# Performance work log

Measured on AMD Instinct MI355X. Metric: run time of the kernel, lower is better.

Reference implementation:

```python
import jax, jax.numpy as jnp
import numpy as np

# ---- config (from init_kwargs) ----
PRE_NMS_THRESH = 0.05
PRE_NMS_TOP_N = 1000
NMS_THRESH = 0.6
FPN_POST_NMS_TOP_N = 100
MIN_SIZE = 0.0
FPN_STRIDES = (8.0, 16.0, 32.0, 64.0, 128.0)
TO_REMOVE = 1.0

M = 2097152   # total FPN points over the batch
N = 16        # images
C = 11        # classes incl. background column (zeroed)


def setup_inputs() -> dict:
    key = jax.random.key(0)
    k1, k2, k3, k4, k5, k6 = jax.random.split(key, 6)
    locations = jax.random.uniform(k1, (M, 2), jnp.float32) * 1024.0
    box_cls = jax.random.normal(k2, (M, C), jnp.float32) * 2.0
    box_regression = jax.random.uniform(k3, (M, 4), jnp.float32) * 4.0
    centerness = jax.random.normal(k4, (M, 1), jnp.float32)
    levels = jax.random.randint(k5, (M,), 0, len(FPN_STRIDES), jnp.int32)
    batch_indices = jnp.sort(jax.random.randint(k6, (M,), 0, N, jnp.int32))
    image_sizes = jnp.tile(jnp.array([[800, 1333]], jnp.int32), (N, 1))  # (h, w)
    return dict(locations=locations, levels=levels, batch_indices=batch_indices,
                box_cls=box_cls, box_regression=box_regression,
                centerness=centerness, image_sizes=image_sizes)


def _iou_matrix(b):
    x1, y1, x2, y2 = b[:, 0], b[:, 1], b[:, 2], b[:, 3]
    area = jnp.clip(x2 - x1 + TO_REMOVE, 0.0) * jnp.clip(y2 - y1 + TO_REMOVE, 0.0)
    xx1 = jnp.maximum(x1[:, None], x1[None, :])
    yy1 = jnp.maximum(y1[:, None], y1[None, :])
    xx2 = jnp.minimum(x2[:, None], x2[None, :])
    yy2 = jnp.minimum(y2[:, None], y2[None, :])
    inter = jnp.clip(xx2 - xx1 + TO_REMOVE, 0.0) * jnp.clip(yy2 - yy1 + TO_REMOVE, 0.0)
    return inter / jnp.maximum(area[:, None] + area[None, :] - inter, 1e-9)


def _greedy_nms(iou, keep0):
    # boxes assumed sorted by descending score; keep0 = validity mask
    K = keep0.shape[0]
    idx = jnp.arange(K)
    def step(keep, i):
        sup = (iou[i] > NMS_THRESH) & (idx > i) & keep[i]
        return keep & ~sup, None
    keep, _ = jax.lax.scan(step, keep0, jnp.arange(K))
    return keep


def _fcos_post(locations, box_cls, box_regression, centerness,
               levels, batch_indices, image_sizes):
    strides = jnp.asarray(FPN_STRIDES, box_regression.dtype)
    reg = box_regression * strides[levels][:, None]          # norm_reg_targets=True
    scores = jax.nn.sigmoid(box_cls) * jax.nn.sigmoid(centerness)  # [M,C]
    scores = scores.at[:, -1].set(0.0)                       # kill background column
    boxes_all = jnp.concatenate([locations - reg[:, :2],
                                 locations + reg[:, 2:]], axis=-1)  # [M,4]

    def per_image(args):
        i, hw = args
        m = (batch_indices == i)[:, None] & (scores > PRE_NMS_THRESH)
        flat = jnp.where(m, scores, 0.0).reshape(-1)          # [M*C]
        topv, topi = jax.lax.top_k(flat, PRE_NMS_TOP_N)       # sorted desc
        pt = topi // C
        cl = (topi % C + 1).astype(jnp.int32)                 # labels = class + 1
        b = boxes_all[pt]                                     # [K,4]
        v0 = topv > 0.0                                       # pad entries -> invalid
        sc = jnp.sqrt(jnp.where(v0, topv, 1.0)) * v0          # sqrt(score), safe at pads
        h = hw[0].astype(b.dtype); w = hw[1].astype(b.dtype)
        x1 = jnp.clip(b[:, 0], 0.0, w - TO_REMOVE)            # clip_to_image
        y1 = jnp.clip(b[:, 1], 0.0, h - TO_REMOVE)
        x2 = jnp.clip(b[:, 2], 0.0, w - TO_REMOVE)
        y2 = jnp.clip(b[:, 3], 0.0, h - TO_REMOVE)
        b = jnp.stack([x1, y1, x2, y2], axis=-1)
        ws = x2 - x1 + TO_REMOVE; hs = y2 - y1 + TO_REMOVE    # remove_small_boxes
        keep0 = v0 & (ws >= MIN_SIZE) & (hs >= MIN_SIZE)
        # class-aware NMS via coordinate offset trick
        max_coord = jnp.max(jnp.where(keep0[:, None], b, 0.0))
        boff = jax.lax.stop_gradient(b + (cl.astype(b.dtype) * (max_coord + 1.0))[:, None])
        keep = _greedy_nms(_iou_matrix(boff), keep0)
        sck = jnp.where(keep, sc, 0.0)
        fv, fi = jax.lax.top_k(sck, FPN_POST_NMS_TOP_N)       # fpn_post_nms_top_n
        return b[fi], fv, cl[fi], fv > 0.0

    boxes_o, scores_o, labels_o, valid_o = jax.lax.map(
        per_image, (jnp.arange(N), image_sizes))
    return boxes_o, scores_o, labels_o, valid_o


def reference(locations, levels, batch_indices, box_cls, box_regression,
              centerness, image_sizes):
    return _fcos_post(locations, box_cls, box_regression, centerness,
                      levels, batch_indices, image_sizes)
```

## Files before the change

kernel.cpp:

```cpp
#include <hip/hip_runtime.h>
#include <math.h>

#pragma clang fp contract(off)

#define MPTS   2097152
#define NIMG   16
#define NCLS   11
#define CUTB   0x3F000000u
#define PREB   0x3F4CCC00u
#define BSAFE  620
#define PRECAP 14336
#define NB2    1026
#define NB2P   1040
#define MARG   96u
#define CAP    4096
#define TOPN   1000
#define OUTN   100
#define LCAP   64

typedef unsigned long long u64;

#define SUPW_PER_IMG 8704
__device__ __forceinline__ int chunk_base(int c) {
    return 64 * (16 * c - (c * (c - 1)) / 2);
}

__device__ inline float sigx(float x) {
    float e = (float)exp(-(double)x);
    return 1.0f / (1.0f + e);
}
__device__ inline float sigf(float x) {
    float e = __expf(-x);
    return __builtin_amdgcn_rcpf(1.0f + e);
}
__device__ inline float bfr(float x) {
    unsigned u = __float_as_uint(x);
    unsigned r = (u + 0x7FFFu + ((u >> 16) & 1u)) & 0xFFFF0000u;
    return __uint_as_float(r);
}
__device__ __forceinline__ u64 rdlane64(u64 v, int l) {
    unsigned lo = (unsigned)__builtin_amdgcn_readlane((int)(unsigned)(v & 0xFFFFFFFFull), l);
    unsigned hi = (unsigned)__builtin_amdgcn_readlane((int)(unsigned)(v >> 32), l);
    return ((u64)hi << 32) | (u64)lo;
}

__global__ __launch_bounds__(1024)
void k_hist(const float4* __restrict__ cls4, const float* __restrict__ ctr,
            const int* __restrict__ batch, unsigned* __restrict__ ghist,
            unsigned* __restrict__ gcnt, unsigned* __restrict__ prerec) {
    __shared__ unsigned hist[NB2];
    __shared__ unsigned pA[512], pB[256];
    __shared__ unsigned cA, cB, bA;
    __shared__ int simg;
    const int F4  = MPTS * NCLS / 4;
    const int FPB = F4 / 512;
    int f0 = blockIdx.x * FPB;
    int t = threadIdx.x;
    for (int i = t; i < NB2; i += 1024) hist[i] = 0;
    if (t == 0) { simg = batch[(unsigned)(4u * (unsigned)f0) / NCLS]; cA = 0; cB = 0; }
    __syncthreads();
    int bi = simg;
    unsigned pc = 0xFFFFFFFFu;
    float sfc = 0.0f;
    int bc = 0;
    for (int f = f0 + t; f < f0 + FPB; f += 1024) {
        float4 v = cls4[f];
        float va[4] = {v.x, v.y, v.z, v.w};
        unsigned e0 = 4u * (unsigned)f;
        #pragma unroll
        for (int j = 0; j < 4; j++) {
            float ck = va[j];
            if (ck <= 0.0f) continue;
            unsigned e = e0 + (unsigned)j;
            unsigned p = e / NCLS;
            unsigned k = e - p * NCLS;
            if (k == 10u) continue;
            if (p != pc) {
                pc = p; sfc = sigf(ctr[p]); bc = batch[p];
            }
            unsigned fb = __float_as_uint(sigf(ck) * sfc);
            if (fb < CUTB) continue;
            unsigned bin = (fb - CUTB) >> 13;
            if (bin >= NB2) bin = NB2 - 1;
            if (bc == bi) atomicAdd(&hist[bin], 1u);
            else          atomicAdd(&ghist[(size_t)bc * NB2P + bin], 1u);
            if (fb >= PREB) {
                if (bc == bi) {
                    unsigned sl = atomicAdd(&cA, 1u);
                    if (sl < 512u) pA[sl] = e;
                    else {
                        unsigned pos = atomicAdd(&gcnt[bi * 16 + 8], 1u);
                        if (pos < PRECAP) prerec[(size_t)bi * PRECAP + pos] = e;
                    }
                } else {
                    unsigned sl = atomicAdd(&cB, 1u);
                    if (sl < 256u) pB[sl] = e;
                    else {
                        unsigned pos = atomicAdd(&gcnt[bc * 16 + 8], 1u);
                        if (pos < PRECAP) prerec[(size_t)bc * PRECAP + pos] = e;
                    }
                }
            }
        }
    }
    __syncthreads();
    unsigned* gh = ghist + (size_t)bi * NB2P;
    for (int i = t; i < NB2; i += 1024) {
        unsigned v2 = hist[i];
        if (v2) atomicAdd(&gh[i], v2);
    }
    if (t == 0) {
        unsigned nn = cA; if (nn > 512u) nn = 512u;
        cA = nn;
        bA = nn ? atomicAdd(&gcnt[bi * 16 + 8], nn) : 0u;
    }
    __syncthreads();
    for (unsigned i = t; i < cA; i += 1024) {
        unsigned pos = bA + i;
        if (pos < PRECAP) prerec[(size_t)bi * PRECAP + pos] = pA[i];
    }
    unsigned nb = cB; if (nb > 256u) nb = 256u;
    for (unsigned i = t; i < nb; i += 1024) {
        unsigned e2 = pB[i];
        int img2 = batch[e2 / NCLS];
        unsigned pos = atomicAdd(&gcnt[img2 * 16 + 8], 1u);
        if (pos < PRECAP) prerec[(size_t)img2 * PRECAP + pos] = e2;
    }
}

__global__ void k_thresh(const unsigned* __restrict__ ghist, unsigned* __restrict__ thrbuf,
                         unsigned* __restrict__ gcnt) {
    int img = blockIdx.x;
    const unsigned* h = ghist + (size_t)img * NB2P;
    __shared__ unsigned psum[256];
    int t = threadIdx.x;
    unsigned s = 0;
    int base = t * 5;
    for (int i = 0; i < 5; i++) { int b = base + i; if (b < NB2) s += h[b]; }
    psum[t] = s;
    __syncthreads();
    if (t == 0) {
        unsigned run = 0; int B = 0;
        for (int u = 205; u >= 0; u--) {
            if (run + psum[u] >= (unsigned)TOPN) {
                int btop = u * 5 + 4; if (btop > NB2 - 1) btop = NB2 - 1;
                for (int b = btop; b >= u * 5; b--) {
                    run += h[b];
                    if (run >= (unsigned)TOPN) { B = b; break; }
                }
                break;
            }
            run += psum[u];
        }
        unsigned TB = CUTB + ((unsigned)B << 13) - MARG;
        thrbuf[2 * img] = TB;
        thrbuf[2 * img + 1] = __float_as_uint(__uint_as_float(TB) * 0.998f);
        if (B < BSAFE || gcnt[img * 16 + 8] > PRECAP) atomicOr(&gcnt[1], 1u);
    }
}

__global__ __launch_bounds__(256)
void k_collect(const float4* __restrict__ cls4, const float* __restrict__ clsf,
               const float* __restrict__ ctr, const int* __restrict__ batch,
               const unsigned* __restrict__ thrbuf, unsigned* __restrict__ gcnt,
               const unsigned* __restrict__ prerec, unsigned long long* __restrict__ cand) {
    int t = threadIdx.x;
    if (gcnt[1] == 0u) {
        if (blockIdx.x >= 256) return;
        int img = blockIdx.x >> 4;
        int sub = blockIdx.x & 15;
        unsigned TB = thrbuf[2 * img];
        float scr = __uint_as_float(thrbuf[2 * img + 1]);
        unsigned n = gcnt[img * 16 + 8];
        __shared__ u64 l2[512];
        __shared__ unsigned c2, b2;
        if (t == 0) c2 = 0;
        __syncthreads();
        const unsigned* pr = prerec + (size_t)img * PRECAP;
        for (unsigned i = (unsigned)(sub * 256 + t); i < n; i += 4096) {
            unsigned e = pr[i];
            unsigned p = e / NCLS;
            float ck = clsf[e];
            float cgs = ctr[p];
            float sf = sigf(ck) * sigf(cgs);
            if (sf > scr) {
                float s = sigx(ck) * sigx(cgs);
                unsigned bits = __float_as_uint(s);
                if (bits >= TB && s > 0.05f) {
                    u64 key = ((u64)bits << 32) | (u64)(0xFFFFFFFFu - e);
                    unsigned sl = atomicAdd(&c2, 1u);
                    if (sl < 512u) l2[sl] = key;
                    else {
                        unsigned pos = atomicAdd(&gcnt[img * 16], 1u);
                        if (pos < CAP) cand[(size_t)img * CAP + pos] = key;
                    }
                }
            }
        }
        __syncthreads();
        if (t == 0) {
            unsigned nn = c2; if (nn > 512u) nn = 512u;
            c2 = nn;
            b2 = nn ? atomicAdd(&gcnt[img * 16], nn) : 0u;
        }
        __syncthreads();
        for (unsigned sl = t; sl < c2; sl += 256) {
            unsigned pos = b2 + sl;
            if (pos < CAP) cand[(size_t)img * CAP + pos] = l2[sl];
        }
        return;
    }
    __shared__ unsigned sTB[NIMG];
    __shared__ float sSCR[NIMG];
    __shared__ u64 lbuf[NIMG][LCAP];
    __shared__ unsigned lcnt[NIMG];
    __shared__ unsigned lbase[NIMG];
    if (t < NIMG) {
        sTB[t]  = thrbuf[2 * t];
        sSCR[t] = __uint_as_float(thrbuf[2 * t + 1]);
        lcnt[t] = 0;
    }
    __syncthreads();
    const int F4  = MPTS * NCLS / 4;
    const int FPB = F4 / 2048;
    int f0 = blockIdx.x * FPB;
    unsigned pc = 0xFFFFFFFFu;
    float cgs = 0.0f, sfc = 0.0f, sxc = 0.0f, scrc = 0.0f;
    bool havex = false;
    int bc = 0; unsigned TBc = 0;
    for (int f = f0 + t; f < f0 + FPB; f += 256) {
        float4 v = cls4[f];
        float va[4] = {v.x, v.y, v.z, v.w};
        unsigned e0 = 4u * (unsigned)f;
        #pragma unroll
        for (int j = 0; j < 4; j++) {
            float ck = va[j];
            if (ck <= -0.001f) continue;
            unsigned e = e0 + (unsigned)j;
            unsigned p = e / NCLS;
            unsigned k = e - p * NCLS;
            if (k == 10u) continue;
            if (p != pc) {
                pc = p; cgs = ctr[p]; bc = batch[p];
                sfc = sigf(cgs); havex = false;
                TBc = sTB[bc]; scrc = sSCR[bc];
            }
            float sf = sigf(ck) * sfc;
            if (sf > scrc) {
                if (!havex) { sxc = sigx(cgs); havex = true; }
                float s = sigx(ck) * sxc;
                unsigned bits = __float_as_uint(s);
                if (bits >= TBc && s > 0.05f) {
                    u64 key = ((u64)bits << 32) | (u64)(0xFFFFFFFFu - e);
                    unsigned slot = atomicAdd(&lcnt[bc], 1u);
                    if (slot < LCAP) lbuf[bc][slot] = key;
                    else {
                        unsigned pos = atomicAdd(&gcnt[bc * 16], 1u);
                        if (pos < CAP) cand[(size_t)bc * CAP + pos] = key;
                    }
                }
            }
        }
    }
    __syncthreads();
    if (t < NIMG) {
        unsigned n = lcnt[t]; if (n > LCAP) n = LCAP;
        lcnt[t] = n;
        lbase[t] = n ? atomicAdd(&gcnt[t * 16], n) : 0u;
    }
    __syncthreads();
    for (int s = t; s < NIMG * LCAP; s += 256) {
        int im = s >> 6;
        int sl = s & (LCAP - 1);
        if (sl < (int)lcnt[im]) {
            unsigned pos = lbase[im] + (unsigned)sl;
            if (pos < CAP) cand[(size_t)im * CAP + pos] = lbuf[im][sl];
        }
    }
}

__global__ __launch_bounds__(1024)
void k_rankb(const u64* __restrict__ cand, const unsigned* __restrict__ gcnt,
             const float* __restrict__ loc, const float* __restrict__ breg,
             const int* __restrict__ levels, const int* __restrict__ imsz,
             float* __restrict__ bx, float* __restrict__ sc, int* __restrict__ cl,
             unsigned* __restrict__ k0, float* __restrict__ bo, float* __restrict__ ar) {
    int img = blockIdx.x;
    int t = threadIdx.x;
    __shared__ u64 keys[CAP];
    __shared__ u64 srtl[TOPN];
    __shared__ float red[1024];
    __shared__ float smc;
    unsigned n = gcnt[img * 16]; if (n > CAP) n = CAP;
    for (int i = t; i < (int)n; i += 1024) keys[i] = cand[(size_t)img * CAP + i];
    for (int i = t; i < TOPN; i += 1024) srtl[i] = 0ull;
    __syncthreads();
    for (int ii = t; ii < (int)n; ii += 1024) {
        u64 me = keys[ii];
        int rank = 0;
        int j = 0;
        for (; j + 4 <= (int)n; j += 4) {
            rank += (keys[j]     > me);
            rank += (keys[j + 1] > me);
            rank += (keys[j + 2] > me);
            rank += (keys[j + 3] > me);
        }
        for (; j < (int)n; j++) rank += (keys[j] > me);
        if (rank < TOPN) srtl[rank] = me;
    }
    __syncthreads();
    float wmax = (float)imsz[img * 2 + 1] - 1.0f;
    float hmax = (float)imsz[img * 2 + 0] - 1.0f;
    float lmax = 0.0f;
    for (int r = t; r < TOPN; r += 1024) {
        u64 kv = srtl[r];
        unsigned bits = (unsigned)(kv >> 32);
        unsigned idx = 0xFFFFFFFFu - (unsigned)(kv & 0xFFFFFFFFull);
        float v = __uint_as_float(bits);
        bool v0 = (kv != 0ull) && (v > 0.0f);
        if (!v0) idx = 0;
        unsigned pt = idx / NCLS;
        int c = (int)(idx - pt * NCLS);
        float lx = loc[(size_t)pt * 2 + 0], ly = loc[(size_t)pt * 2 + 1];
        float st = (float)(8 << levels[pt]);
        float r0 = breg[(size_t)pt * 4 + 0] * st;
        float r1 = breg[(size_t)pt * 4 + 1] * st;
        float r2 = breg[(size_t)pt * 4 + 2] * st;
        float r3 = breg[(size_t)pt * 4 + 3] * st;
        float x1 = lx - r0, y1 = ly - r1, x2 = lx + r2, y2 = ly + r3;
        x1 = fminf(fmaxf(x1, 0.0f), wmax);
        y1 = fminf(fmaxf(y1, 0.0f), hmax);
        x2 = fminf(fmaxf(x2, 0.0f), wmax);
        y2 = fminf(fmaxf(y2, 0.0f), hmax);
        float wss = (x2 - x1) + 1.0f, hss = (y2 - y1) + 1.0f;
        bool keep = v0 && (wss >= 0.0f) && (hss >= 0.0f);
        size_t ob = (size_t)img * TOPN + r;
        bx[ob * 4 + 0] = x1; bx[ob * 4 + 1] = y1;
        bx[ob * 4 + 2] = x2; bx[ob * 4 + 3] = y2;
        sc[ob] = v0 ? sqrtf(v) : 0.0f;
        cl[ob] = c + 1;
        k0[ob] = keep ? 1u : 0u;
        if (keep) lmax = fmaxf(lmax, fmaxf(fmaxf(x1, y1), fmaxf(x2, y2)));
    }
    red[t] = lmax; __syncthreads();
    for (int sft = 512; sft > 0; sft >>= 1) {
        if (t < sft) red[t] = fmaxf(red[t], red[t + sft]);
        __syncthreads();
    }
    if (t == 0) smc = red[0];
    __syncthreads();
    float off1 = smc + 1.0f;
    for (int r = t; r < TOPN; r += 1024) {
        size_t ob = (size_t)img * TOPN + r;
        float o = (float)cl[ob] * off1;
        float x1 = bx[ob * 4 + 0] + o, y1 = bx[ob * 4 + 1] + o;
        float x2 = bx[ob * 4 + 2] + o, y2 = bx[ob * 4 + 3] + o;
        bo[ob * 4 + 0] = x1; bo[ob * 4 + 1] = y1;
        bo[ob * 4 + 2] = x2; bo[ob * 4 + 3] = y2;
        float aw = fmaxf((x2 - x1) + 1.0f, 0.0f);
        float ah = fmaxf((y2 - y1) + 1.0f, 0.0f);
        ar[ob] = aw * ah;
    }
}

__global__ __launch_bounds__(1024)
void k_iou(const float* __restrict__ bo, const float* __restrict__ ar,
           u64* __restrict__ sup) {
    int img = blockIdx.x >> 4;
    int c   = blockIdx.x & 15;
    __shared__ float sx1[1024], sy1[1024], sx2[1024], sy2[1024], sa[1024];
    int tid = threadIdx.x;
    {
        int i = tid;
        if (i < TOPN) {
            size_t ob = (size_t)img * TOPN + i;
            sx1[i] = bo[ob * 4 + 0]; sy1[i] = bo[ob * 4 + 1];
            sx2[i] = bo[ob * 4 + 2]; sy2[i] = bo[ob * 4 + 3];
            sa[i]  = ar[ob];
        } else {
            sx1[i] = 0.0f; sy1[i] = 0.0f; sx2[i] = 0.0f; sy2[i] = 0.0f; sa[i] = 0.0f;
        }
    }
    __syncthreads();
    int width = 16 - c;
    int items = 64 * width;
    u64* supc = sup + (size_t)img * SUPW_PER_IMG + chunk_base(c);
    for (int it = tid; it < items; it += 1024) {
        int r  = it & 63;
        int wq = c + (it >> 6);
        int i  = c * 64 + r;
        if (i >= TOPN) continue;
        float x1 = sx1[i], y1 = sy1[i], x2 = sx2[i], y2 = sy2[i], a = sa[i];
        int j0 = wq * 64;
        u64 m = 0ull;
        #pragma unroll 8
        for (int jj = 0; jj < 64; jj++) {
            int j = j0 + jj;
            float xx1 = fmaxf(x1, sx1[j]);
            float yy1 = fmaxf(y1, sy1[j]);
            float xx2 = fminf(x2, sx2[j]);
            float yy2 = fminf(y2, sy2[j]);
            float iw = fmaxf((xx2 - xx1) + 1.0f, 0.0f);
            float ih = fmaxf((yy2 - yy1) + 1.0f, 0.0f);
            float inter = iw * ih;
            float den = fmaxf((a + sa[j]) - inter, 1e-9f);
            if (inter / den > 0.6f) m |= (1ull << jj);
        }
        u64 vm = ~0ull;
        if (wq == c) vm = (r >= 63) ? 0ull : (~0ull << (r + 1));
        int rem = TOPN - j0;
        if (rem < 64) vm &= (rem <= 0) ? 0ull : ((1ull << rem) - 1ull);
        supc[(size_t)r * width + (wq - c)] = m & vm;
    }
}

__device__ __forceinline__ void scan_pref(const u64* __restrict__ supi, int rg, int w, int t,
                                          int C, u64 (&V)[16], u64 &anyV, u64 &dmy) {
    int wd = 16 - C;
    const u64* rb = supi + chunk_base(C) + (rg << 4) * wd - C + w;
    u64 a = 0ull;
    #pragma unroll
    for (int i = 0; i < 16; i++) {
        u64 x = rb[i * wd];
        V[i] = (w >= C) ? x : 0ull;
        a |= V[i];
    }
    anyV = a;
    dmy = supi[chunk_base(C) + (size_t)t * wd];
}

__device__ __forceinline__ void scan_step(int rg, int w, int C,
                                          u64 (&V)[16], u64 anyV, u64 dmy,
                                          u64 &kw_local) {
    u64 m = rdlane64(kw_local, C);
    u64 act = __ballot(dmy != 0ull) & m;
    while (act) {
        int r = __builtin_ctzll(act);
        u64 d = rdlane64(dmy, r);
        m &= ~d;
        act &= act - 1ull;
        act &= m;
    }
    if (__ballot(anyV != 0ull)) {
        u64 loc = 0ull;
        #pragma unroll
        for (int i = 0; i < 16; i++) {
            int row = (rg << 4) + i;
            loc |= V[i] & ((u64)0 - ((m >> row) & 1ull));
        }
        u64 t1 = loc | __shfl_xor(loc, 16);
        u64 t2 = t1 | __shfl_xor(t1, 32);
        kw_local = ((w == C) ? m : kw_local) & ~t2;
    } else if (w == C) {
        kw_local = m;
    }
}

__global__ __launch_bounds__(64)
void k_scan_out(const u64* __restrict__ sup, const unsigned* __restrict__ k0,
                const float* __restrict__ bx, const float* __restrict__ sc,
                const int* __restrict__ cl, float* __restrict__ out) {
    int img = blockIdx.x;
    int t = threadIdx.x;
    int rg = t >> 4, w = t & 15;
    const u64* supi = sup + (size_t)img * SUPW_PER_IMG;

    u64 kw_local = 0ull;
    #pragma unroll
    for (int q = 0; q < 16; q++) {
        int i = (q << 6) + t;
        unsigned vv = (i < TOPN) ? k0[(size_t)img * TOPN + i] : 0u;
        u64 bal = __ballot(vv != 0u);
        if (w == q) kw_local = bal;
    }

    u64 vA[16], vB[16], anyA, anyB, dA, dB;
    scan_pref(supi, rg, w, t, 0, vA, anyA, dA);
    for (int c = 0; c < 16; c += 2) {
        scan_pref(supi, rg, w, t, c + 1, vB, anyB, dB);
        scan_step(rg, w, c, vA, anyA, dA, kw_local);
        if (c + 2 < 16) scan_pref(supi, rg, w, t, c + 2, vA, anyA, dA);
        scan_step(rg, w, c + 1, vB, anyB, dB, kw_local);
    }

    u64 kws[16];
    #pragma unroll
    for (int q = 0; q < 16; q++) kws[q] = rdlane64(kw_local, q);

    __shared__ int fi[OUTN];
    int total_k = 0;
    #pragma unroll
    for (int q = 0; q < 16; q++) total_k += __popcll(kws[q]);
    int snk = total_k < OUTN ? total_k : OUTN;
    int run = 0;
    #pragma unroll
    for (int q = 0; q < 16; q++) {
        u64 word = kws[q];
        int i = (q << 6) + t;
        int kb = __popcll(word & ((1ull << t) - 1ull));
        bool kept = ((word >> t) & 1ull) != 0ull;
        int krank = run + kb;
        if (kept) {
            if (krank < OUTN) fi[krank] = i;
        } else if (i < TOPN) {
            int slot = snk + (i - krank);
            if (slot < OUTN) fi[slot] = i;
        }
        run += __popcll(word);
    }
    __syncthreads();

    for (int q = t; q < OUTN; q += 64) {
        int r = fi[q];
        bool kv = q < snk;
        size_t ob = (size_t)img * TOPN + r;
        float sv = kv ? sc[ob] : 0.0f;
        int o = img * OUTN + q;
        out[o * 4 + 0] = bfr(bx[ob * 4 + 0]);
        out[o * 4 + 1] = bfr(bx[ob * 4 + 1]);
        out[o * 4 + 2] = bfr(bx[ob * 4 + 2]);
        out[o * 4 + 3] = bfr(bx[ob * 4 + 3]);
        out[6400 + o] = bfr(sv);
        out[8000 + o] = (float)cl[ob];
        out[9600 + o] = (sv > 0.0f) ? 1.0f : 0.0f;
    }
}

extern "C" void kernel_launch(void* const* d_in, const int* in_sizes, int n_in,
                              void* d_out, int out_size, void* d_ws, size_t ws_size,
                              hipStream_t stream) {
    const float* loc    = (const float*)d_in[0];
    const int*   levels = (const int*)d_in[1];
    const int*   batch  = (const int*)d_in[2];
    const float* cls    = (const float*)d_in[3];
    const float* breg   = (const float*)d_in[4];
    const float* ctr    = (const float*)d_in[5];
    const int*   imsz   = (const int*)d_in[6];

    char* ws = (char*)d_ws;
    unsigned long long* cand   = (unsigned long long*)(ws + 0);
    unsigned*           ghist  = (unsigned*)(ws + 524288);
    float*              bx     = (float*)(ws + 852096);
    float*              bo     = (float*)(ws + 1108096);
    float*              ar     = (float*)(ws + 1364096);
    float*              sc     = (float*)(ws + 1428096);
    int*                cl     = (int*)(ws + 1492096);
    unsigned*           k0     = (unsigned*)(ws + 1556096);
    unsigned*           gcnt   = (unsigned*)(ws + 1620096);
    unsigned*           thrbuf = (unsigned*)(ws + 1621120);
    u64*                sup    = (u64*)(ws + 1703936);
    unsigned*           prerec = (unsigned*)(ws + 1703936);
    float* out = (float*)d_out;

    hipMemsetAsync(ghist, 0, 16 * NB2P * 4, stream);
    hipMemsetAsync(gcnt, 0, 1024, stream);
    k_hist    <<<512,  1024, 0, stream>>>((const float4*)cls, ctr, batch, ghist, gcnt, prerec);
    k_thresh  <<<16,   256,  0, stream>>>(ghist, thrbuf, gcnt);
    k_collect <<<2048, 256,  0, stream>>>((const float4*)cls, cls, ctr, batch, thrbuf, gcnt, prerec, cand);
    k_rankb   <<<16,   1024, 0, stream>>>(cand, gcnt, loc, breg, levels, imsz,
                                          bx, sc, cl, k0, bo, ar);
    k_iou     <<<256,  1024, 0, stream>>>(bo, ar, sup);
    k_scan_out<<<16,   64,   0, stream>>>(sup, k0, bx, sc, cl, out);
}
```

Baseline: 303.3 us.

## Fuse post-histogram stages into fewer kernels and add centerness-based early reject

```diff
diff --git a/kernel.cpp b/kernel.cpp
--- a/kernel.cpp
+++ b/kernel.cpp
@@ -16,7 +16,6 @@
 #define CAP    4096
 #define TOPN   1000
 #define OUTN   100
-#define LCAP   64
 
 typedef unsigned long long u64;
 
@@ -61,7 +60,8 @@
     __syncthreads();
     int bi = simg;
     unsigned pc = 0xFFFFFFFFu;
-    float sfc = 0.0f;
+    unsigned bcp = 0xFFFFFFFFu;
+    float sfc = 0.0f, Tm = 3.0e38f;
     int bc = 0;
     for (int f = f0 + t; f < f0 + FPB; f += 1024) {
         float4 v = cls4[f];
@@ -69,19 +69,29 @@
         unsigned e0 = 4u * (unsigned)f;
         #pragma unroll
         for (int j = 0; j < 4; j++) {
-            float ck = va[j];
-            if (ck <= 0.0f) continue;
             unsigned e = e0 + (unsigned)j;
             unsigned p = e / NCLS;
             unsigned k = e - p * NCLS;
             if (k == 10u) continue;
             if (p != pc) {
-                pc = p; sfc = sigf(ctr[p]); bc = batch[p];
-            }
+                pc = p;
+                float c = ctr[p];
+                if (c > 0.0f) {
+                    float q = sigf(c);
+                    sfc = q;
+                    Tm = (q > 0.50001f) ? (-0.6931472f - __logf(q - 0.5f) - 0.02f)
+                                        : -3.0e38f;
+                } else {
+                    Tm = 3.0e38f; sfc = 0.0f;
+                }
+            }
+            float ck = va[j];
+            if (!(ck > Tm)) continue;
             unsigned fb = __float_as_uint(sigf(ck) * sfc);
             if (fb < CUTB) continue;
             unsigned bin = (fb - CUTB) >> 13;
             if (bin >= NB2) bin = NB2 - 1;
+            if (p != bcp) { bcp = p; bc = batch[p]; }
             if (bc == bi) atomicAdd(&hist[bin], 1u);
             else          atomicAdd(&ghist[(size_t)bc * NB2P + bin], 1u);
             if (fb >= PREB) {
@@ -128,54 +138,60 @@
     }
 }
 
-__global__ void k_thresh(const unsigned* __restrict__ ghist, unsigned* __restrict__ thrbuf,
-                         unsigned* __restrict__ gcnt) {
-    int img = blockIdx.x;
-    const unsigned* h = ghist + (size_t)img * NB2P;
+__global__ __launch_bounds__(256)
+void k_collect(const float* __restrict__ clsf, const float* __restrict__ ctr,
+               const int* __restrict__ batch, const unsigned* __restrict__ ghist,
+               unsigned* __restrict__ gcnt, const unsigned* __restrict__ prerec,
+               unsigned long long* __restrict__ cand) {
+    int t = threadIdx.x;
+    int img = blockIdx.x >> 4;
+    int sub = blockIdx.x & 15;
     __shared__ unsigned psum[256];
-    int t = threadIdx.x;
-    unsigned s = 0;
-    int base = t * 5;
-    for (int i = 0; i < 5; i++) { int b = base + i; if (b < NB2) s += h[b]; }
-    psum[t] = s;
-    __syncthreads();
-    if (t == 0) {
-        unsigned run = 0; int B = 0;
-        for (int u = 205; u >= 0; u--) {
-            if (run + psum[u] >= (unsigned)TOPN) {
-                int btop = u * 5 + 4; if (btop > NB2 - 1) btop = NB2 - 1;
-                for (int b = btop; b >= u * 5; b--) {
-                    run += h[b];
-                    if (run >= (unsigned)TOPN) { B = b; break; }
-                }
-                break;
-            }
-            run += psum[u];
-        }
-        unsigned TB = CUTB + ((unsigned)B << 13) - MARG;
-        thrbuf[2 * img] = TB;
-        thrbuf[2 * img + 1] = __float_as_uint(__uint_as_float(TB) * 0.998f);
-        if (B < BSAFE || gcnt[img * 16 + 8] > PRECAP) atomicOr(&gcnt[1], 1u);
-    }
-}
-
-__global__ __launch_bounds__(256)
-void k_collect(const float4* __restrict__ cls4, const float* __restrict__ clsf,
-               const float* __restrict__ ctr, const int* __restrict__ batch,
-               const unsigned* __restrict__ thrbuf, unsigned* __restrict__ gcnt,
-               const unsigned* __restrict__ prerec, unsigned long long* __restrict__ cand) {
-    int t = threadIdx.x;
-    if (gcnt[1] == 0u) {
-        if (blockIdx.x >= 256) return;
-        int img = blockIdx.x >> 4;
-        int sub = blockIdx.x & 15;
-        unsigned TB = thrbuf[2 * img];
-        float scr = __uint_as_float(thrbuf[2 * img + 1]);
-        unsigned n = gcnt[img * 16 + 8];
-        __shared__ u64 l2[512];
-        __shared__ unsigned c2, b2;
+    __shared__ unsigned sTB;
+    __shared__ float sSCR;
+    __shared__ int sSAFE, sPlo, sPhi;
+    __shared__ u64 l2[512];
+    __shared__ unsigned c2, b2;
+    {
+        const unsigned* h = ghist + (size_t)img * NB2P;
+        unsigned s = 0;
+        int base = t * 5;
+        for (int i = 0; i < 5; i++) { int b = base + i; if (b < NB2) s += h[b]; }
+        psum[t] = s;
         if (t == 0) c2 = 0;
         __syncthreads();
+        if (t == 0) {
+            unsigned run = 0; int B = 0;
+            for (int u = 205; u >= 0; u--) {
+                if (run + psum[u] >= (unsigned)TOPN) {
+                    int btop = u * 5 + 4; if (btop > NB2 - 1) btop = NB2 - 1;
+                    for (int b = btop; b >= u * 5; b--) {
+                        run += h[b];
+                        if (run >= (unsigned)TOPN) { B = b; break; }
+                    }
+                    break;
+                }
+                run += psum[u];
+            }
+            unsigned TB = CUTB + ((unsigned)B << 13) - MARG;
+            sTB = TB;
+            sSCR = __uint_as_float(TB) * 0.998f;
+            sSAFE = (B >= BSAFE && gcnt[img * 16 + 8] <= PRECAP) ? 1 : 0;
+            if (!sSAFE) {
+                int lo = 0, hi = MPTS;
+                while (lo < hi) { int m = (lo + hi) >> 1; if (batch[m] < img) lo = m + 1; else hi = m; }
+                sPlo = lo;
+                int lo2 = lo, hi2 = MPTS;
+                while (lo2 < hi2) { int m = (lo2 + hi2) >> 1; if (batch[m] < img + 1) lo2 = m + 1; else hi2 = m; }
+                sPhi = lo2;
+            }
+        }
+        __syncthreads();
+    }
+    unsigned TB = sTB;
+    float scr = sSCR;
+    if (sSAFE) {
+        unsigned n = gcnt[img * 16 + 8];
         const unsigned* pr = prerec + (size_t)img * PRECAP;
         for (unsigned i = (unsigned)(sub * 256 + t); i < n; i += 4096) {
             unsigned e = pr[i];
@@ -208,112 +224,118 @@
             unsigned pos = b2 + sl;
             if (pos < CAP) cand[(size_t)img * CAP + pos] = l2[sl];
         }
-        return;
-    }
-    __shared__ unsigned sTB[NIMG];
-    __shared__ float sSCR[NIMG];
-    __shared__ u64 lbuf[NIMG][LCAP];
-    __shared__ unsigned lcnt[NIMG];
-    __shared__ unsigned lbase[NIMG];
-    if (t < NIMG) {
-        sTB[t]  = thrbuf[2 * t];
-        sSCR[t] = __uint_as_float(thrbuf[2 * t + 1]);
-        lcnt[t] = 0;
-    }
-    __syncthreads();
-    const int F4  = MPTS * NCLS / 4;
-    const int FPB = F4 / 2048;
-    int f0 = blockIdx.x * FPB;
-    unsigned pc = 0xFFFFFFFFu;
-    float cgs = 0.0f, sfc = 0.0f, sxc = 0.0f, scrc = 0.0f;
-    bool havex = false;
-    int bc = 0; unsigned TBc = 0;
-    for (int f = f0 + t; f < f0 + FPB; f += 256) {
-        float4 v = cls4[f];
-        float va[4] = {v.x, v.y, v.z, v.w};
-        unsigned e0 = 4u * (unsigned)f;
-        #pragma unroll
-        for (int j = 0; j < 4; j++) {
-            float ck = va[j];
-            if (ck <= -0.001f) continue;
-            unsigned e = e0 + (unsigned)j;
+    } else {
+        long total_e = (long)(sPhi - sPlo) * NCLS;
+        long ebase = (long)sPlo * NCLS;
+        for (long idx = sub * 256 + t; idx < total_e; idx += 4096) {
+            unsigned e = (unsigned)(ebase + idx);
             unsigned p = e / NCLS;
             unsigned k = e - p * NCLS;
             if (k == 10u) continue;
-            if (p != pc) {
-                pc = p; cgs = ctr[p]; bc = batch[p];
-                sfc = sigf(cgs); havex = false;
-                TBc = sTB[bc]; scrc = sSCR[bc];
-            }
-            float sf = sigf(ck) * sfc;
-            if (sf > scrc) {
-                if (!havex) { sxc = sigx(cgs); havex = true; }
-                float s = sigx(ck) * sxc;
+            float ck = clsf[e];
+            if (ck <= -0.001f) continue;
+            float cgs = ctr[p];
+            float sf = sigf(ck) * sigf(cgs);
+            if (sf > scr) {
+                float s = sigx(ck) * sigx(cgs);
                 unsigned bits = __float_as_uint(s);
-                if (bits >= TBc && s > 0.05f) {
+                if (bits >= TB && s > 0.05f) {
                     u64 key = ((u64)bits << 32) | (u64)(0xFFFFFFFFu - e);
-                    unsigned slot = atomicAdd(&lcnt[bc], 1u);
-                    if (slot < LCAP) lbuf[bc][slot] = key;
-                    else {
-                        unsigned pos = atomicAdd(&gcnt[bc * 16], 1u);
-                        if (pos < CAP) cand[(size_t)bc * CAP + pos] = key;
-                    }
+                    unsigned pos = atomicAdd(&gcnt[img * 16], 1u);
+                    if (pos < CAP) cand[(size_t)img * CAP + pos] = key;
                 }
             }
         }
     }
-    __syncthreads();
-    if (t < NIMG) {
-        unsigned n = lcnt[t]; if (n > LCAP) n = LCAP;
-        lcnt[t] = n;
-        lbase[t] = n ? atomicAdd(&gcnt[t * 16], n) : 0u;
-    }
-    __syncthreads();
-    for (int s = t; s < NIMG * LCAP; s += 256) {
-        int im = s >> 6;
-        int sl = s & (LCAP - 1);
-        if (sl < (int)lcnt[im]) {
-            unsigned pos = lbase[im] + (unsigned)sl;
-            if (pos < CAP) cand[(size_t)im * CAP + pos] = lbuf[im][sl];
-        }
-    }
-}
+}
+
+__device__ __forceinline__ void scan_pref(const u64* supi, int rg, int w, int t,
+                                          int C, u64 (&V)[16], u64 &anyV, u64 &dmy) {
+    int wd = 16 - C;
+    const u64* rb = supi + chunk_base(C) + (rg << 4) * wd - C + w;
+    u64 a = 0ull;
+    #pragma unroll
+    for (int i = 0; i < 16; i++) {
+        u64 x = rb[i * wd];
+        V[i] = (w >= C) ? x : 0ull;
+        a |= V[i];
+    }
+    anyV = a;
+    dmy = supi[chunk_base(C) + (size_t)t * wd];
+}
+
+__device__ __forceinline__ void scan_step(int rg, int w, int C,
+                                          u64 (&V)[16], u64 anyV, u64 dmy,
+                                          u64 &kw_local) {
+    u64 m = rdlane64(kw_local, C);
+    u64 act = __ballot(dmy != 0ull) & m;
+    while (act) {
+        int r = __builtin_ctzll(act);
+        u64 d = rdlane64(dmy, r);
+        m &= ~d;
+        act &= act - 1ull;
+        act &= m;
+    }
+    if (__ballot(anyV != 0ull)) {
+        u64 loc = 0ull;
+        #pragma unroll
+        for (int i = 0; i < 16; i++) {
+            int row = (rg << 4) + i;
+            loc |= V[i] & ((u64)0 - ((m >> row) & 1ull));
+        }
+        u64 t1 = loc | __shfl_xor(loc, 16);
+        u64 t2 = t1 | __shfl_xor(t1, 32);
+        kw_local = ((w == C) ? m : kw_local) & ~t2;
+    } else if (w == C) {
+        kw_local = m;
+    }
+}
+
+struct RankBufs { u64 keys[CAP]; u64 srtl[TOPN]; };
+union BackU { RankBufs r; u64 supL[SUPW_PER_IMG]; };
 
 __global__ __launch_bounds__(1024)
-void k_rankb(const u64* __restrict__ cand, const unsigned* __restrict__ gcnt,
-             const float* __restrict__ loc, const float* __restrict__ breg,
-             const int* __restrict__ levels, const int* __restrict__ imsz,
-             float* __restrict__ bx, float* __restrict__ sc, int* __restrict__ cl,
-             unsigned* __restrict__ k0, float* __restrict__ bo, float* __restrict__ ar) {
+void k_back(const u64* __restrict__ cand, const unsigned* __restrict__ gcnt,
+            const float* __restrict__ loc, const float* __restrict__ breg,
+            const int* __restrict__ levels, const int* __restrict__ imsz,
+            float* __restrict__ out) {
     int img = blockIdx.x;
     int t = threadIdx.x;
-    __shared__ u64 keys[CAP];
-    __shared__ u64 srtl[TOPN];
+    __shared__ BackU uA;
+    __shared__ float sx1[1024], sy1[1024], sx2[1024], sy2[1024], sa2[1024];
+    __shared__ float bxl[TOPN * 4];
+    __shared__ float scl[TOPN];
+    __shared__ int   cll[TOPN];
+    __shared__ unsigned char k0l[1024];
     __shared__ float red[1024];
     __shared__ float smc;
+    __shared__ int fi[OUTN];
+    __shared__ int snkS;
+
     unsigned n = gcnt[img * 16]; if (n > CAP) n = CAP;
-    for (int i = t; i < (int)n; i += 1024) keys[i] = cand[(size_t)img * CAP + i];
-    for (int i = t; i < TOPN; i += 1024) srtl[i] = 0ull;
+    for (int i = t; i < (int)n; i += 1024) uA.r.keys[i] = cand[(size_t)img * CAP + i];
+    if (t < TOPN) uA.r.srtl[t] = 0ull;
     __syncthreads();
     for (int ii = t; ii < (int)n; ii += 1024) {
-        u64 me = keys[ii];
+        u64 me = uA.r.keys[ii];
         int rank = 0;
         int j = 0;
         for (; j + 4 <= (int)n; j += 4) {
-            rank += (keys[j]     > me);
-            rank += (keys[j + 1] > me);
-            rank += (keys[j + 2] > me);
-            rank += (keys[j + 3] > me);
-        }
-        for (; j < (int)n; j++) rank += (keys[j] > me);
-        if (rank < TOPN) srtl[rank] = me;
-    }
-    __syncthreads();
+            rank += (uA.r.keys[j]     > me);
+            rank += (uA.r.keys[j + 1] > me);
+            rank += (uA.r.keys[j + 2] > me);
+            rank += (uA.r.keys[j + 3] > me);
+        }
+        for (; j < (int)n; j++) rank += (uA.r.keys[j] > me);
+        if (rank < TOPN) uA.r.srtl[rank] = me;
+    }
+    __syncthreads();
+
     float wmax = (float)imsz[img * 2 + 1] - 1.0f;
     float hmax = (float)imsz[img * 2 + 0] - 1.0f;
     float lmax = 0.0f;
-    for (int r = t; r < TOPN; r += 1024) {
-        u64 kv = srtl[r];
+    if (t < TOPN) {
+        u64 kv = uA.r.srtl[t];
         unsigned bits = (unsigned)(kv >> 32);
         unsigned idx = 0xFFFFFFFFu - (unsigned)(kv & 0xFFFFFFFFull);
         float v = __uint_as_float(bits);
@@ -334,12 +356,11 @@
         y2 = fminf(fmaxf(y2, 0.0f), hmax);
         float wss = (x2 - x1) + 1.0f, hss = (y2 - y1) + 1.0f;
         bool keep = v0 && (wss >= 0.0f) && (hss >= 0.0f);
-        size_t ob = (size_t)img * TOPN + r;
-        bx[ob * 4 + 0] = x1; bx[ob * 4 + 1] = y1;
-        bx[ob * 4 + 2] = x2; bx[ob * 4 + 3] = y2;
-        sc[ob] = v0 ? sqrtf(v) : 0.0f;
-        cl[ob] = c + 1;
-        k0[ob] = keep ? 1u : 0u;
+        bxl[t * 4 + 0] = x1; bxl[t * 4 + 1] = y1;
+        bxl[t * 4 + 2] = x2; bxl[t * 4 + 3] = y2;
+        scl[t] = v0 ? sqrtf(v) : 0.0f;
+        cll[t] = c + 1;
+        k0l[t] = keep ? 1 : 0;
         if (keep) lmax = fmaxf(lmax, fmaxf(fmaxf(x1, y1), fmaxf(x2, y2)));
     }
     red[t] = lmax; __syncthreads();
@@ -350,178 +371,107 @@
     if (t == 0) smc = red[0];
     __syncthreads();
     float off1 = smc + 1.0f;
-    for (int r = t; r < TOPN; r += 1024) {
-        size_t ob = (size_t)img * TOPN + r;
-        float o = (float)cl[ob] * off1;
-        float x1 = bx[ob * 4 + 0] + o, y1 = bx[ob * 4 + 1] + o;
-        float x2 = bx[ob * 4 + 2] + o, y2 = bx[ob * 4 + 3] + o;
-        bo[ob * 4 + 0] = x1; bo[ob * 4 + 1] = y1;
-        bo[ob * 4 + 2] = x2; bo[ob * 4 + 3] = y2;
+    if (t < TOPN) {
+        float o = (float)cll[t] * off1;
+        float x1 = bxl[t * 4 + 0] + o, y1 = bxl[t * 4 + 1] + o;
+        float x2 = bxl[t * 4 + 2] + o, y2 = bxl[t * 4 + 3] + o;
+        sx1[t] = x1; sy1[t] = y1; sx2[t] = x2; sy2[t] = y2;
         float aw = fmaxf((x2 - x1) + 1.0f, 0.0f);
         float ah = fmaxf((y2 - y1) + 1.0f, 0.0f);
-        ar[ob] = aw * ah;
-    }
-}
-
-__global__ __launch_bounds__(1024)
-void k_iou(const float* __restrict__ bo, const float* __restrict__ ar,
-           u64* __restrict__ sup) {
-    int img = blockIdx.x >> 4;
-    int c   = blockIdx.x & 15;
-    __shared__ float sx1[1024], sy1[1024], sx2[1024], sy2[1024], sa[1024];
-    int tid = threadIdx.x;
-    {
-        int i = tid;
-        if (i < TOPN) {
-            size_t ob = (size_t)img * TOPN + i;
-            sx1[i] = bo[ob * 4 + 0]; sy1[i] = bo[ob * 4 + 1];
-            sx2[i] = bo[ob * 4 + 2]; sy2[i] = bo[ob * 4 + 3];
-            sa[i]  = ar[ob];
-        } else {
-            sx1[i] = 0.0f; sy1[i] = 0.0f; sx2[i] = 0.0f; sy2[i] = 0.0f; sa[i] = 0.0f;
-        }
-    }
-    __syncthreads();
-    int width = 16 - c;
-    int items = 64 * width;
-    u64* supc = sup + (size_t)img * SUPW_PER_IMG + chunk_base(c);
-    for (int it = tid; it < items; it += 1024) {
-        int r  = it & 63;
-        int wq = c + (it >> 6);
-        int i  = c * 64 + r;
-        if (i >= TOPN) continue;
-        float x1 = sx1[i], y1 = sy1[i], x2 = sx2[i], y2 = sy2[i], a = sa[i];
-        int j0 = wq * 64;
-        u64 m = 0ull;
-        #pragma unroll 8
-        for (int jj = 0; jj < 64; jj++) {
-            int j = j0 + jj;
-            float xx1 = fmaxf(x1, sx1[j]);
-            float yy1 = fmaxf(y1, sy1[j]);
-            float xx2 = fminf(x2, sx2[j]);
-            float yy2 = fminf(y2, sy2[j]);
-            float iw = fmaxf((xx2 - xx1) + 1.0f, 0.0f);
-            float ih = fmaxf((yy2 - yy1) + 1.0f, 0.0f);
-            float inter = iw * ih;
-            float den = fmaxf((a + sa[j]) - inter, 1e-9f);
-            if (inter / den > 0.6f) m |= (1ull << jj);
-        }
-        u64 vm = ~0ull;
-        if (wq == c) vm = (r >= 63) ? 0ull : (~0ull << (r + 1));
-        int rem = TOPN - j0;
-        if (rem < 64) vm &= (rem <= 0) ? 0ull : ((1ull << rem) - 1ull);
-        supc[(size_t)r * width + (wq - c)] = m & vm;
-    }
-}
-
-__device__ __forceinline__ void scan_pref(const u64* __restrict__ supi, int rg, int w, int t,
-                                          int C, u64 (&V)[16], u64 &anyV, u64 &dmy) {
-    int wd = 16 - C;
-    const u64* rb = supi + chunk_base(C) + (rg << 4) * wd - C + w;
-    u64 a = 0ull;
-    #pragma unroll
-    for (int i = 0; i < 16; i++) {
-        u64 x = rb[i * wd];
-        V[i] = (w >= C) ? x : 0ull;
-        a |= V[i];
-    }
-    anyV = a;
-    dmy = supi[chunk_base(C) + (size_t)t * wd];
-}
-
-__device__ __forceinline__ void scan_step(int rg, int w, int C,
-                                          u64 (&V)[16], u64 anyV, u64 dmy,
-                                          u64 &kw_local) {
-    u64 m = rdlane64(kw_local, C);
-    u64 act = __ballot(dmy != 0ull) & m;
-    while (act) {
-        int r = __builtin_ctzll(act);
-        u64 d = rdlane64(dmy, r);
-        m &= ~d;
-        act &= act - 1ull;
-        act &= m;
-    }
-    if (__ballot(anyV != 0ull)) {
-        u64 loc = 0ull;
+        sa2[t] = aw * ah;
+    } else {
+        sx1[t] = 0.0f; sy1[t] = 0.0f; sx2[t] = 0.0f; sy2[t] = 0.0f; sa2[t] = 0.0f;
+    }
+    __syncthreads();
+
+    for (int c = 0; c < 16; c++) {
+        int width = 16 - c;
+        int items = 64 * width;
+        u64* supc = uA.supL + chunk_base(c);
+        for (int it = t; it < items; it += 1024) {
+            int r  = it & 63;
+            int wq = c + (it >> 6);
+            int i  = c * 64 + r;
+            if (i >= TOPN) continue;
+            float x1 = sx1[i], y1 = sy1[i], x2 = sx2[i], y2 = sy2[i], a = sa2[i];
+            int j0 = wq * 64;
+            u64 m = 0ull;
+            #pragma unroll 8
+            for (int jj = 0; jj < 64; jj++) {
+                int j = j0 + jj;
+                float xx1 = fmaxf(x1, sx1[j]);
+                float yy1 = fmaxf(y1, sy1[j]);
+                float xx2 = fminf(x2, sx2[j]);
+                float yy2 = fminf(y2, sy2[j]);
+                float iw = fmaxf((xx2 - xx1) + 1.0f, 0.0f);
+                float ih = fmaxf((yy2 - yy1) + 1.0f, 0.0f);
+                float inter = iw * ih;
+                float den = fmaxf((a + sa2[j]) - inter, 1e-9f);
+                if (inter / den > 0.6f) m |= (1ull << jj);
+            }
+            u64 vm = ~0ull;
+            if (wq == c) vm = (r >= 63) ? 0ull : (~0ull << (r + 1));
+            int rem = TOPN - j0;
+            if (rem < 64) vm &= (rem <= 0) ? 0ull : ((1ull << rem) - 1ull);
+            supc[(size_t)r * width + (wq - c)] = m & vm;
+        }
+    }
+    __syncthreads();
+
+    if (t < 64) {
+        int rg = t >> 4, w = t & 15;
+        const u64* supi = uA.supL;
+        u64 kw_local = 0ull;
         #pragma unroll
-        for (int i = 0; i < 16; i++) {
-            int row = (rg << 4) + i;
-            loc |= V[i] & ((u64)0 - ((m >> row) & 1ull));
-        }
-        u64 t1 = loc | __shfl_xor(loc, 16);
-        u64 t2 = t1 | __shfl_xor(t1, 32);
-        kw_local = ((w == C) ? m : kw_local) & ~t2;
-    } else if (w == C) {
-        kw_local = m;
-    }
-}
-
-__global__ __launch_bounds__(64)
-void k_scan_out(const u64* __restrict__ sup, const unsigned* __restrict__ k0,
-                const float* __restrict__ bx, const float* __restrict__ sc,
-                const int* __restrict__ cl, float* __restrict__ out) {
-    int img = blockIdx.x;
-    int t = threadIdx.x;
-    int rg = t >> 4, w = t & 15;
-    const u64* supi = sup + (size_t)img * SUPW_PER_IMG;
-
-    u64 kw_local = 0ull;
-    #pragma unroll
-    for (int q = 0; q < 16; q++) {
-        int i = (q << 6) + t;
-        unsigned vv = (i < TOPN) ? k0[(size_t)img * TOPN + i] : 0u;
-        u64 bal = __ballot(vv != 0u);
-        if (w == q) kw_local = bal;
-    }
-
-    u64 vA[16], vB[16], anyA, anyB, dA, dB;
-    scan_pref(supi, rg, w, t, 0, vA, anyA, dA);
-    for (int c = 0; c < 16; c += 2) {
-        scan_pref(supi, rg, w, t, c + 1, vB, anyB, dB);
-        scan_step(rg, w, c, vA, anyA, dA, kw_local);
-        if (c + 2 < 16) scan_pref(supi, rg, w, t, c + 2, vA, anyA, dA);
-        scan_step(rg, w, c + 1, vB, anyB, dB, kw_local);
-    }
-
-    u64 kws[16];
-    #pragma unroll
-    for (int q = 0; q < 16; q++) kws[q] = rdlane64(kw_local, q);
-
-    __shared__ int fi[OUTN];
-    int total_k = 0;
-    #pragma unroll
-    for (int q = 0; q < 16; q++) total_k += __popcll(kws[q]);
-    int snk = total_k < OUTN ? total_k : OUTN;
-    int run = 0;
-    #pragma unroll
-    for (int q = 0; q < 16; q++) {
-        u64 word = kws[q];
-        int i = (q << 6) + t;
-        int kb = __popcll(word & ((1ull << t) - 1ull));
-        bool kept = ((word >> t) & 1ull) != 0ull;
-        int krank = run + kb;
-        if (kept) {
-            if (krank < OUTN) fi[krank] = i;
-        } else if (i < TOPN) {
-            int slot = snk + (i - krank);
-            if (slot < OUTN) fi[slot] = i;
-        }
-        run += __popcll(word);
-    }
-    __syncthreads();
-
-    for (int q = t; q < OUTN; q += 64) {
-        int r = fi[q];
-        bool kv = q < snk;
-        size_t ob = (size_t)img * TOPN + r;
-        float sv = kv ? sc[ob] : 0.0f;
-        int o = img * OUTN + q;
-        out[o * 4 + 0] = bfr(bx[ob * 4 + 0]);
-        out[o * 4 + 1] = bfr(bx[ob * 4 + 1]);
-        out[o * 4 + 2] = bfr(bx[ob * 4 + 2]);
-        out[o * 4 + 3] = bfr(bx[ob * 4 + 3]);
+        for (int q = 0; q < 16; q++) {
+            int i = (q << 6) + t;
+            unsigned vv = (i < TOPN) ? (unsigned)k0l[i] : 0u;
+            u64 bal = __ballot(vv != 0u);
+            if (w == q) kw_local = bal;
+        }
+        u64 V[16], anyV, dmy;
+        for (int c = 0; c < 16; c++) {
+            scan_pref(supi, rg, w, t, c, V, anyV, dmy);
+            scan_step(rg, w, c, V, anyV, dmy, kw_local);
+        }
+        u64 kws[16];
+        #pragma unroll
+        for (int q = 0; q < 16; q++) kws[q] = rdlane64(kw_local, q);
+        int total_k = 0;
+        #pragma unroll
+        for (int q = 0; q < 16; q++) total_k += __popcll(kws[q]);
+        int snk = total_k < OUTN ? total_k : OUTN;
+        int run = 0;
+        #pragma unroll
+        for (int q = 0; q < 16; q++) {
+            u64 word = kws[q];
+            int i = (q << 6) + t;
+            int kb = __popcll(word & ((1ull << t) - 1ull));
+            bool kept = ((word >> t) & 1ull) != 0ull;
+            int krank = run + kb;
+            if (kept) {
+                if (krank < OUTN) fi[krank] = i;
+            } else if (i < TOPN) {
+                int slot = snk + (i - krank);
+                if (slot < OUTN) fi[slot] = i;
+            }
+            run += __popcll(word);
+        }
+        if (t == 0) snkS = snk;
+    }
+    __syncthreads();
+
+    if (t < OUTN) {
+        int r = fi[t];
+        bool kv = t < snkS;
+        float sv = kv ? scl[r] : 0.0f;
+        int o = img * OUTN + t;
+        out[o * 4 + 0] = bfr(bxl[r * 4 + 0]);
+        out[o * 4 + 1] = bfr(bxl[r * 4 + 1]);
+        out[o * 4 + 2] = bfr(bxl[r * 4 + 2]);
+        out[o * 4 + 3] = bfr(bxl[r * 4 + 3]);
         out[6400 + o] = bfr(sv);
-        out[8000 + o] = (float)cl[ob];
+        out[8000 + o] = (float)cll[r];
         out[9600 + o] = (sv > 0.0f) ? 1.0f : 0.0f;
     }
 }
@@ -540,25 +490,12 @@
     char* ws = (char*)d_ws;
     unsigned long long* cand   = (unsigned long long*)(ws + 0);
     unsigned*           ghist  = (unsigned*)(ws + 524288);
-    float*              bx     = (float*)(ws + 852096);
-    float*              bo     = (float*)(ws + 1108096);
-    float*              ar     = (float*)(ws + 1364096);
-    float*              sc     = (float*)(ws + 1428096);
-    int*                cl     = (int*)(ws + 1492096);
-    unsigned*           k0     = (unsigned*)(ws + 1556096);
-    unsigned*           gcnt   = (unsigned*)(ws + 1620096);
-    unsigned*           thrbuf = (unsigned*)(ws + 1621120);
-    u64*                sup    = (u64*)(ws + 1703936);
+    unsigned*           gcnt   = (unsigned*)(ws + 590848);
     unsigned*           prerec = (unsigned*)(ws + 1703936);
     float* out = (float*)d_out;
 
-    hipMemsetAsync(ghist, 0, 16 * NB2P * 4, stream);
-    hipMemsetAsync(gcnt, 0, 1024, stream);
-    k_hist    <<<512,  1024, 0, stream>>>((const float4*)cls, ctr, batch, ghist, gcnt, prerec);
-    k_thresh  <<<16,   256,  0, stream>>>(ghist, thrbuf, gcnt);
-    k_collect <<<2048, 256,  0, stream>>>((const float4*)cls, cls, ctr, batch, thrbuf, gcnt, prerec, cand);
-    k_rankb   <<<16,   1024, 0, stream>>>(cand, gcnt, loc, breg, levels, imsz,
-                                          bx, sc, cl, k0, bo, ar);
-    k_iou     <<<256,  1024, 0, stream>>>(bo, ar, sup);
-    k_scan_out<<<16,   64,   0, stream>>>(sup, k0, bx, sc, cl, out);
-}
+    hipMemsetAsync(ghist, 0, 66560 + 1024, stream);
+    k_hist    <<<512, 1024, 0, stream>>>((const float4*)cls, ctr, batch, ghist, gcnt, prerec);
+    k_collect <<<256, 256,  0, stream>>>(cls, ctr, batch, ghist, gcnt, prerec, cand);
+    k_back    <<<16,  1024, 0, stream>>>(cand, gcnt, loc, breg, levels, imsz, out);
+}
```

Result: slower. 417.4 us (+37.6%).
